# Optimization experiments

Hardware: AMD Instinct MI355X
Metric: run time of the kernel (lower is better)

The kernel has to match this reference:

```python
import jax, jax.numpy as jnp
import numpy as np

N_NODES = 100000
N_EDGES = 3200000
DROP_P = 0.5


def gcn_conv(x, W, b, src, dst, deg_inv_sqrt, n):
    # PyG GCNConv with self-loops already folded into (src, dst):
    # out[j] = sum_{(i->j)} dinv[i]*dinv[j] * (x W)[i] + b
    h = x @ W
    norm = deg_inv_sqrt[src] * deg_inv_sqrt[dst]          # [E+N]
    msg = h[src] * norm[:, None]                          # [E+N, d_out]
    out = jax.ops.segment_sum(msg, dst, num_segments=n)
    return out + b


def dropout(x, key, p=DROP_P):
    keep = jax.random.bernoulli(key, 1.0 - p, x.shape)
    return jnp.where(keep, x / (1.0 - p), 0.0)


def setup_inputs() -> dict:
    key = jax.random.key(0)
    ks = jax.random.split(key, 8)
    x = jax.random.normal(ks[0], (N_NODES, 64), dtype=jnp.float32)
    edge_index = jax.random.randint(ks[1], (2, N_EDGES), 0, N_NODES, dtype=jnp.int64)
    def glorot(k, fin, fout):
        lim = float(np.sqrt(6.0 / (fin + fout)))
        return jax.random.uniform(k, (fin, fout), jnp.float32, -lim, lim)
    return {
        "x": x,
        "edge_index": edge_index,
        "W1": glorot(ks[2], 64, 32), "b1": jnp.zeros((32,), jnp.float32),
        "W2": glorot(ks[3], 32, 64), "b2": jnp.zeros((64,), jnp.float32),
        "W3": glorot(ks[4], 64, 32), "b3": jnp.zeros((32,), jnp.float32),
    }


def reference(x, edge_index, W1, b1, W2, b2, W3, b3):
    n = x.shape[0]
    loops = jnp.arange(n, dtype=edge_index.dtype)
    src = jnp.concatenate([edge_index[0], loops])          # [E+N]
    dst = jnp.concatenate([edge_index[1], loops])
    deg = jax.ops.segment_sum(jnp.ones_like(dst, dtype=x.dtype), dst, num_segments=n)
    deg_inv_sqrt = jnp.where(deg > 0, jax.lax.rsqrt(deg), 0.0)

    dkey = jax.random.key(42)
    k1, k2 = jax.random.split(dkey)

    h = gcn_conv(x, W1, b1, src, dst, deg_inv_sqrt, n)
    h = jax.nn.celu(h)
    h = dropout(h, k1)
    h = gcn_conv(h, W2, b2, src, dst, deg_inv_sqrt, n)
    h = jax.nn.celu(h)
    h = dropout(h, k2)
    h = gcn_conv(h, W3, b3, src, dst, deg_inv_sqrt, n)
    return jax.nn.celu(h)
```

## Files before the change

### kernel.cpp

```cpp
#include <hip/hip_runtime.h>
#include <stdint.h>
#include <stddef.h>

typedef _Float16 half_t;
typedef _Float16 half4 __attribute__((ext_vector_type(4)));
typedef _Float16 half8 __attribute__((ext_vector_type(8)));

__host__ __device__ __forceinline__ uint32_t rotl32(uint32_t v, uint32_t r) {
  return (v << r) | (v >> (32u - r));
}

__host__ __device__ __forceinline__ void tf2x32(uint32_t k0, uint32_t k1,
                                                uint32_t x0, uint32_t x1,
                                                uint32_t& o0, uint32_t& o1) {
  uint32_t ks2 = k0 ^ k1 ^ 0x1BD11BDAu;
  x0 += k0; x1 += k1;
  x0 += x1; x1 = rotl32(x1, 13); x1 ^= x0;
  x0 += x1; x1 = rotl32(x1, 15); x1 ^= x0;
  x0 += x1; x1 = rotl32(x1, 26); x1 ^= x0;
  x0 += x1; x1 = rotl32(x1, 6);  x1 ^= x0;
  x0 += k1; x1 += ks2 + 1u;
  x0 += x1; x1 = rotl32(x1, 17); x1 ^= x0;
  x0 += x1; x1 = rotl32(x1, 29); x1 ^= x0;
  x0 += x1; x1 = rotl32(x1, 16); x1 ^= x0;
  x0 += x1; x1 = rotl32(x1, 24); x1 ^= x0;
  x0 += ks2; x1 += k0 + 2u;
  x0 += x1; x1 = rotl32(x1, 13); x1 ^= x0;
  x0 += x1; x1 = rotl32(x1, 15); x1 ^= x0;
  x0 += x1; x1 = rotl32(x1, 26); x1 ^= x0;
  x0 += x1; x1 = rotl32(x1, 6);  x1 ^= x0;
  x0 += k0; x1 += k1 + 3u;
  x0 += x1; x1 = rotl32(x1, 17); x1 ^= x0;
  x0 += x1; x1 = rotl32(x1, 29); x1 ^= x0;
  x0 += x1; x1 = rotl32(x1, 16); x1 ^= x0;
  x0 += x1; x1 = rotl32(x1, 24); x1 ^= x0;
  x0 += k1; x1 += ks2 + 4u;
  x0 += x1; x1 = rotl32(x1, 13); x1 ^= x0;
  x0 += x1; x1 = rotl32(x1, 15); x1 ^= x0;
  x0 += x1; x1 = rotl32(x1, 26); x1 ^= x0;
  x0 += x1; x1 = rotl32(x1, 6);  x1 ^= x0;
  x0 += ks2; x1 += k0 + 5u;
  o0 = x0; o1 = x1;
}

__device__ __forceinline__ bool tf_keep(uint32_t k0, uint32_t k1, uint32_t idx) {
  uint32_t o0, o1;
  tf2x32(k0, k1, 0u, idx, o0, o1);
  return ((o0 ^ o1) >> 31) == 0u;
}

#define CHUNK 4096
#define STASH 5120

__global__ __launch_bounds__(1024) void zero1024(uint32_t* __restrict__ p) {
  p[threadIdx.x] = 0u;
}

__global__ __launch_bounds__(256) void k4_binhist(const int* __restrict__ src,
                                                  const int* __restrict__ dst,
                                                  uint32_t* __restrict__ tbl,
                                                  uint32_t* __restrict__ gbcnt,
                                                  uint32_t* __restrict__ staging,
                                                  int E, int NB) {
  __shared__ uint32_t lcur[1024];
  __shared__ uint32_t ls[256];
  __shared__ uint32_t stage[CHUNK];
  int tid = threadIdx.x;
  for (int i = tid; i < NB; i += 256) lcur[i] = 0u;
  __syncthreads();
  int base = blockIdx.x * CHUNK;
  int end = min(base + CHUNK, E);
  uint32_t dv[16], sv[16];
  int m = 0;
  for (int i = base + tid; i < end; i += 256) {
    dv[m] = (uint32_t)dst[i];
    sv[m] = (uint32_t)src[i];
    ++m;
  }
  for (int q = 0; q < m; ++q) atomicAdd(&lcur[dv[q] >> 7], 1u);
  __syncthreads();
  uint32_t carry = 0u;
  for (int seg = 0; seg < 1024; seg += 256) {
    int i = seg + tid;
    uint32_t v = (i < NB) ? lcur[i] : 0u;
    ls[tid] = v;
    __syncthreads();
    for (int off = 1; off < 256; off <<= 1) {
      uint32_t t = (tid >= off) ? ls[tid - off] : 0u;
      __syncthreads();
      if (tid >= off) ls[tid] += t;
      __syncthreads();
    }
    uint32_t excl = carry + ls[tid] - v;
    if (i < NB) {
      tbl[(size_t)blockIdx.x * NB + i] = (excl << 16) | v;
      if (v) atomicAdd(&gbcnt[i], v);
      lcur[i] = excl;
    }
    carry += ls[255];
    __syncthreads();
  }
  for (int q = 0; q < m; ++q) {
    uint32_t d = dv[q];
    uint32_t p = atomicAdd(&lcur[d >> 7], 1u);
    stage[p] = ((d & 127u) << 17) | sv[q];
  }
  __syncthreads();
  int cnt_total = end - base;
  uint32_t* outp = staging + (size_t)blockIdx.x * CHUNK;
  for (int i = tid; i < cnt_total; i += 256) outp[i] = stage[i];
}

__global__ __launch_bounds__(1024) void k3_bscan(const uint32_t* __restrict__ gbcnt,
                                                 uint32_t* __restrict__ bbase, int NB) {
  __shared__ uint32_t s[1024];
  int i = threadIdx.x;
  uint32_t v = (i < NB) ? gbcnt[i] : 0u;
  s[i] = v;
  __syncthreads();
  for (int off = 1; off < 1024; off <<= 1) {
    uint32_t t = (i >= off) ? s[i - off] : 0u;
    __syncthreads();
    if (i >= off) s[i] += t;
    __syncthreads();
  }
  if (i < NB) bbase[i] = s[i] - v;
}

__global__ __launch_bounds__(256) void k5_fin(
    const uint32_t* __restrict__ staging, const uint32_t* __restrict__ tbl,
    const uint32_t* __restrict__ bbase, uint32_t* __restrict__ rowp,
    float* __restrict__ dinv, uint32_t* __restrict__ esrc,
    int n, int E, int NBLK, int NB) {
  __shared__ uint32_t lpak[1024];
  __shared__ uint32_t P[1025];
  __shared__ uint32_t ls[256];
  __shared__ uint32_t stash[STASH];
  __shared__ uint32_t lc[128];
  __shared__ uint32_t sc[128];
  __shared__ uint32_t lcur[128];
  int tid = threadIdx.x;
  int b = blockIdx.x;
  if (tid < 128) lc[tid] = 0u;
  uint32_t carry = 0u;
  for (int seg = 0; seg < 1024; seg += 256) {
    int i = seg + tid;
    uint32_t packed = (i < NBLK) ? tbl[(size_t)i * NB + b] : 0u;
    lpak[i] = packed;
    uint32_t v = packed & 0xFFFFu;
    ls[tid] = v;
    __syncthreads();
    for (int off = 1; off < 256; off <<= 1) {
      uint32_t t = (tid >= off) ? ls[tid - off] : 0u;
      __syncthreads();
      if (tid >= off) ls[tid] += t;
      __syncthreads();
    }
    P[i] = carry + ls[tid] - v;
    carry += ls[255];
    __syncthreads();
  }
  if (tid == 0) P[NBLK] = carry;
  __syncthreads();
  uint32_t total = P[NBLK];
  for (int i = tid; i < NBLK; i += 256) {
    uint32_t packed = lpak[i];
    uint32_t cnt = packed & 0xFFFFu;
    uint32_t loff = packed >> 16;
    uint32_t p = P[i];
    const uint32_t* run = staging + (size_t)i * CHUNK + loff;
    for (uint32_t t2 = 0; t2 < cnt; ++t2) {
      uint32_t e = run[t2];
      uint32_t q = p + t2;
      if (q < STASH) stash[q] = e;
      atomicAdd(&lc[e >> 17], 1u);
    }
  }
  __syncthreads();
  uint32_t myc = (tid < 128) ? lc[tid] : 0u;
  if (tid < 128) sc[tid] = myc;
  __syncthreads();
  for (int off = 1; off < 128; off <<= 1) {
    uint32_t t = (tid < 128 && tid >= off) ? sc[tid - off] : 0u;
    __syncthreads();
    if (tid < 128 && tid >= off) sc[tid] += t;
    __syncthreads();
  }
  uint32_t s = bbase[b];
  if (tid < 128) {
    uint32_t gstart = s + sc[tid] - myc;
    int node = (b << 7) + tid;
    if (node < n) {
      rowp[node] = gstart;
      dinv[node] = 1.0f / sqrtf((float)(myc + 1u));
    }
    lcur[tid] = gstart;
  }
  if (b == 0 && tid == 0) rowp[n] = (uint32_t)E;
  __syncthreads();
  uint32_t lim = total < (uint32_t)STASH ? total : (uint32_t)STASH;
  for (uint32_t q = tid; q < lim; q += 256) {
    uint32_t e = stash[q];
    uint32_t pos = atomicAdd(&lcur[e >> 17], 1u);
    esrc[pos] = e & 0x1FFFFu;
  }
  if (total > (uint32_t)STASH) {
    for (int i = tid; i < NBLK; i += 256) {
      uint32_t packed = lpak[i];
      uint32_t cnt = packed & 0xFFFFu;
      uint32_t loff = packed >> 16;
      uint32_t p = P[i];
      const uint32_t* run = staging + (size_t)i * CHUNK + loff;
      for (uint32_t t2 = 0; t2 < cnt; ++t2) {
        uint32_t q = p + t2;
        if (q >= (uint32_t)STASH) {
          uint32_t e = run[t2];
          uint32_t pos = atomicAdd(&lcur[e >> 17], 1u);
          esrc[pos] = e & 0x1FFFFu;
        }
      }
    }
  }
}

__global__ __launch_bounds__(256) void gemm_n64_k32(
    const float* __restrict__ X, const float* __restrict__ W,
    const float* __restrict__ dinv, half_t* __restrict__ out16, int n) {
  __shared__ float Ws[64 * 32];
  __shared__ float Xs[32 * 68];
  int tid = threadIdx.x;
  {
    const float4* Wv = (const float4*)W;
    float4* Wsv = (float4*)Ws;
    Wsv[tid] = Wv[tid];
    Wsv[tid + 256] = Wv[tid + 256];
  }
  int row0 = blockIdx.x * 32;
  {
    const float4* Xv = (const float4*)(X + (size_t)row0 * 64);
    int lim = (n - row0) * 16;
    float4 z = make_float4(0.f, 0.f, 0.f, 0.f);
    int i0 = tid, i1 = tid + 256;
    float4 v0 = (i0 < lim) ? Xv[i0] : z;
    float4 v1 = (i1 < lim) ? Xv[i1] : z;
    *(float4*)(Xs + (i0 >> 4) * 68 + ((i0 & 15) << 2)) = v0;
    *(float4*)(Xs + (i1 >> 4) * 68 + ((i1 & 15) << 2)) = v1;
  }
  __syncthreads();
  int r = tid >> 3;
  int c4 = (tid & 7) << 2;
  int row = row0 + r;
  if (row >= n) return;
  float4 acc = make_float4(0.f, 0.f, 0.f, 0.f);
#pragma unroll
  for (int k = 0; k < 64; k += 4) {
    float4 xv = *(const float4*)(Xs + r * 68 + k);
    float4 w0 = *(const float4*)(Ws + (k + 0) * 32 + c4);
    float4 w1 = *(const float4*)(Ws + (k + 1) * 32 + c4);
    float4 w2 = *(const float4*)(Ws + (k + 2) * 32 + c4);
    float4 w3 = *(const float4*)(Ws + (k + 3) * 32 + c4);
    acc.x = fmaf(xv.x, w0.x, acc.x); acc.y = fmaf(xv.x, w0.y, acc.y);
    acc.z = fmaf(xv.x, w0.z, acc.z); acc.w = fmaf(xv.x, w0.w, acc.w);
    acc.x = fmaf(xv.y, w1.x, acc.x); acc.y = fmaf(xv.y, w1.y, acc.y);
    acc.z = fmaf(xv.y, w1.z, acc.z); acc.w = fmaf(xv.y, w1.w, acc.w);
    acc.x = fmaf(xv.z, w2.x, acc.x); acc.y = fmaf(xv.z, w2.y, acc.y);
    acc.z = fmaf(xv.z, w2.z, acc.z); acc.w = fmaf(xv.z, w2.w, acc.w);
    acc.x = fmaf(xv.w, w3.x, acc.x); acc.y = fmaf(xv.w, w3.y, acc.y);
    acc.z = fmaf(xv.w, w3.z, acc.z); acc.w = fmaf(xv.w, w3.w, acc.w);
  }
  float dj = dinv[row];
  half4 h;
  h.x = (half_t)(acc.x * dj); h.y = (half_t)(acc.y * dj);
  h.z = (half_t)(acc.z * dj); h.w = (half_t)(acc.w * dj);
  *(half4*)(out16 + (size_t)row * 32 + c4) = h;
}

__global__ __launch_bounds__(256) void gemm_k32_n64_act(
    const float* __restrict__ X, const float* __restrict__ W,
    const float* __restrict__ bias, float* __restrict__ out,
    uint32_t k0, uint32_t k1, int n) {
  __shared__ float Ws[32 * 64];
  __shared__ float Xs[16 * 36];
  int tid = threadIdx.x;
  {
    const float4* Wv = (const float4*)W;
    float4* Wsv = (float4*)Ws;
    Wsv[tid] = Wv[tid];
    Wsv[tid + 256] = Wv[tid + 256];
  }
  int row0 = blockIdx.x * 16;
  if (tid < 128) {
    const float4* Xv = (const float4*)(X + (size_t)row0 * 32);
    int lim = (n - row0) * 8;
    float4 z = make_float4(0.f, 0.f, 0.f, 0.f);
    float4 v = (tid < lim) ? Xv[tid] : z;
    *(float4*)(Xs + (tid >> 3) * 36 + ((tid & 7) << 2)) = v;
  }
  __syncthreads();
  int r = tid >> 4;
  int c4 = (tid & 15) << 2;
  int row = row0 + r;
  if (row >= n) return;
  float4 acc = make_float4(0.f, 0.f, 0.f, 0.f);
#pragma unroll
  for (int k = 0; k < 32; k += 4) {
    float4 xv = *(const float4*)(Xs + r * 36 + k);
    float4 w0 = *(const float4*)(Ws + (k + 0) * 64 + c4);
    float4 w1 = *(const float4*)(Ws + (k + 1) * 64 + c4);
    float4 w2 = *(const float4*)(Ws + (k + 2) * 64 + c4);
    float4 w3 = *(const float4*)(Ws + (k + 3) * 64 + c4);
    acc.x = fmaf(xv.x, w0.x, acc.x); acc.y = fmaf(xv.x, w0.y, acc.y);
    acc.z = fmaf(xv.x, w0.z, acc.z); acc.w = fmaf(xv.x, w0.w, acc.w);
    acc.x = fmaf(xv.y, w1.x, acc.x); acc.y = fmaf(xv.y, w1.y, acc.y);
    acc.z = fmaf(xv.y, w1.z, acc.z); acc.w = fmaf(xv.y, w1.w, acc.w);
    acc.x = fmaf(xv.z, w2.x, acc.x); acc.y = fmaf(xv.z, w2.y, acc.y);
    acc.z = fmaf(xv.z, w2.z, acc.z); acc.w = fmaf(xv.z, w2.w, acc.w);
    acc.x = fmaf(xv.w, w3.x, acc.x); acc.y = fmaf(xv.w, w3.y, acc.y);
    acc.z = fmaf(xv.w, w3.z, acc.z); acc.w = fmaf(xv.w, w3.w, acc.w);
  }
  float4 bv = *(const float4*)(bias + c4);
  float vv[4] = {acc.x + bv.x, acc.y + bv.y, acc.z + bv.z, acc.w + bv.w};
  uint32_t base = (uint32_t)row * 64u + (uint32_t)c4;
#pragma unroll
  for (int q = 0; q < 4; ++q) {
    float v = vv[q];
    v = v > 0.f ? v : expm1f(v);
    vv[q] = tf_keep(k0, k1, base + q) ? v * 2.f : 0.f;
  }
  *(float4*)(out + (size_t)row * 64 + c4) = make_float4(vv[0], vv[1], vv[2], vv[3]);
}

__global__ __launch_bounds__(256) void gather_fin(
    const half_t* __restrict__ hs, const uint32_t* __restrict__ rowp,
    const uint32_t* __restrict__ esrc, const float* __restrict__ dinv,
    const float* __restrict__ bias, float* __restrict__ outf,
    half_t* __restrict__ outh, int n, int mode, uint32_t k0, uint32_t k1,
    float fone) {
  __shared__ __align__(16) float ldsred[256];
  int tid = threadIdx.x;
  int gt = blockIdx.x * 256 + tid;
  int j = gt >> 5;
  int g = tid >> 5;
  int l = tid & 31;
  int eslot = l >> 2;
  int chunk = l & 3;
  float acc[8] = {0.f, 0.f, 0.f, 0.f, 0.f, 0.f, 0.f, 0.f};
  uint32_t e0 = 0, deg = 0;
  if (j < n) {
    e0 = rowp[j];
    deg = rowp[j + 1] - e0;
  }
  const half_t* hp = hs + (size_t)(chunk << 3);
  uint32_t base = 0;
  for (; base + 32 <= deg; base += 32) {
    uint32_t idx = esrc[e0 + base + (uint32_t)l];
#pragma unroll
    for (int k = 0; k < 32; k += 8) {
      uint32_t s = (uint32_t)__shfl((int)idx, k + eslot, 32);
      const half8 v = *(const half8*)(hp + ((size_t)s << 5));
#pragma unroll
      for (int q = 0; q < 8; ++q) acc[q] = fmaf((float)v[q], fone, acc[q]);
    }
  }
  if (base < deg) {
    uint32_t rem = deg - base;
    uint32_t li = (uint32_t)l < rem ? (uint32_t)l : rem - 1u;
    uint32_t idx = esrc[e0 + base + li];
    for (uint32_t k = 0; k < rem; k += 8) {
      uint32_t kk = k + (uint32_t)eslot;
      uint32_t ks = kk < rem ? kk : rem - 1u;
      uint32_t s = (uint32_t)__shfl((int)idx, (int)ks, 32);
      if (kk < rem) {
        const half8 v = *(const half8*)(hp + ((size_t)s << 5));
#pragma unroll
        for (int q = 0; q < 8; ++q) acc[q] = fmaf((float)v[q], fone, acc[q]);
      }
    }
  }
#pragma unroll
  for (int m = 4; m <= 16; m <<= 1) {
#pragma unroll
    for (int q = 0; q < 8; ++q) acc[q] += __shfl_xor(acc[q], m);
  }
  if (l < 4) {
    *(float4*)(&ldsred[(g << 5) + (chunk << 3) + 0]) =
        make_float4(acc[0], acc[1], acc[2], acc[3]);
    *(float4*)(&ldsred[(g << 5) + (chunk << 3) + 4]) =
        make_float4(acc[4], acc[5], acc[6], acc[7]);
  }
  __builtin_amdgcn_wave_barrier();
  if (j >= n) return;
  float sum = ldsred[(g << 5) + l];
  sum += (float)hs[(size_t)j * 32 + l];
  float dj = dinv[j];
  float v = dj * sum;
  if (mode == 1) {
    v += bias[l];
    v = v > 0.f ? v : expm1f(v);
    outf[gt] = v;
  } else if (mode == 3) {
    v += bias[l];
    v = v > 0.f ? v : expm1f(v);
    v = tf_keep(k0, k1, (uint32_t)gt) ? v * 2.f : 0.f;
    v *= dj;
    outh[gt] = (half_t)v;
  } else {
    outf[gt] = v;
  }
}

extern "C" void kernel_launch(void* const* d_in, const int* in_sizes, int n_in,
                              void* d_out, int out_size, void* d_ws, size_t ws_size,
                              hipStream_t stream) {
  const float* x  = (const float*)d_in[0];
  const int*   ei = (const int*)d_in[1];
  const float* W1 = (const float*)d_in[2];
  const float* b1 = (const float*)d_in[3];
  const float* W2 = (const float*)d_in[4];
  const float* b2 = (const float*)d_in[5];
  const float* W3 = (const float*)d_in[6];
  const float* b3 = (const float*)d_in[7];
  float* out = (float*)d_out;

  const int n = in_sizes[0] / 64;
  const int E = in_sizes[1] / 2;
  const int* src = ei;
  const int* dst = ei + E;

  char* ws = (char*)d_ws;
  size_t off = 0;
  auto alloc = [&](size_t bytes) {
    void* p = ws + off;
    off = (off + bytes + 255) & ~(size_t)255;
    return p;
  };
  float*    A32   = (float*)alloc((size_t)n * 32 * 4);
  float*    C     = (float*)alloc((size_t)n * 64 * 4);
  half_t*   A16   = (half_t*)alloc((size_t)n * 32 * 2);
  half_t*   B16   = (half_t*)alloc((size_t)n * 32 * 2);
  float*    dinv  = (float*)alloc((size_t)n * 4);
  uint32_t* rowp  = (uint32_t*)alloc((size_t)(n + 1) * 4);
  uint32_t* esrc  = (uint32_t*)alloc((size_t)E * 4);
  uint32_t* gbcnt = (uint32_t*)alloc(1024 * 4);
  uint32_t* bbase = (uint32_t*)alloc(1024 * 4);
  uint32_t* staging = (uint32_t*)C;
  uint32_t* tbl     = (uint32_t*)A32;
  (void)ws_size; (void)n_in; (void)out_size;

  uint32_t k1a, k1b, k2a, k2b;
  tf2x32(0u, 42u, 0u, 0u, k1a, k1b);
  tf2x32(0u, 42u, 0u, 1u, k2a, k2b);

  const int NB   = (n + 127) >> 7;
  const int NBLK = (E + CHUNK - 1) / CHUNK;
  const int nv   = n * 32;
  const int gV   = (nv + 255) / 256;
  const int gG1  = (n + 31) / 32;
  const int gG2  = (n + 15) / 16;
  dim3 blk(256);

  zero1024<<<1, dim3(1024), 0, stream>>>(gbcnt);
  k4_binhist<<<NBLK, blk, 0, stream>>>(src, dst, tbl, gbcnt, staging, E, NB);
  k3_bscan<<<1, dim3(1024), 0, stream>>>(gbcnt, bbase, NB);
  k5_fin<<<NB, blk, 0, stream>>>(staging, tbl, bbase, rowp, dinv, esrc, n, E, NBLK, NB);

  gemm_n64_k32<<<gG1, blk, 0, stream>>>(x, W1, dinv, A16, n);
  gather_fin<<<gV, blk, 0, stream>>>(A16, rowp, esrc, dinv, b1, nullptr, B16, n, 3, k1a, k1b, 1.0f);

  gather_fin<<<gV, blk, 0, stream>>>(B16, rowp, esrc, dinv, nullptr, A32, nullptr, n, 0, 0u, 0u, 1.0f);
  gemm_k32_n64_act<<<gG2, blk, 0, stream>>>(A32, W2, b2, C, k2a, k2b, n);

  gemm_n64_k32<<<gG1, blk, 0, stream>>>(C, W3, dinv, A16, n);
  gather_fin<<<gV, blk, 0, stream>>>(A16, rowp, esrc, dinv, b3, out, nullptr, n, 1, 0u, 0u, 1.0f);
}
```

Before: 334.5 us.

## Widen CSR finalize kernel to 1024 threads with per-edge binary-search gather

The CSR-building finalize kernel now runs 1024 threads per block and does a single 1024-wide prefix scan over chunk counts instead of four 256-wide segmented scans. Edges are no longer copied run by run per chunk. Each thread takes flat edge indices and finds the source chunk with a binary search over the prefix array. This spreads the load evenly across threads and avoids the imbalance from variable run lengths. In exchange it pays a log(NBLK) shared-memory search per edge and assumes NBLK fits in 1024.

```diff
diff --git a/kernel.cpp b/kernel.cpp
--- a/kernel.cpp
+++ b/kernel.cpp
@@ -127,14 +127,14 @@
   if (i < NB) bbase[i] = s[i] - v;
 }
 
-__global__ __launch_bounds__(256) void k5_fin(
+__global__ __launch_bounds__(1024) void k5_fin(
     const uint32_t* __restrict__ staging, const uint32_t* __restrict__ tbl,
     const uint32_t* __restrict__ bbase, uint32_t* __restrict__ rowp,
     float* __restrict__ dinv, uint32_t* __restrict__ esrc,
     int n, int E, int NBLK, int NB) {
-  __shared__ uint32_t lpak[1024];
+  __shared__ uint32_t loff[1024];
   __shared__ uint32_t P[1025];
-  __shared__ uint32_t ls[256];
+  __shared__ uint32_t ls[1024];
   __shared__ uint32_t stash[STASH];
   __shared__ uint32_t lc[128];
   __shared__ uint32_t sc[128];
@@ -142,39 +142,30 @@
   int tid = threadIdx.x;
   int b = blockIdx.x;
   if (tid < 128) lc[tid] = 0u;
-  uint32_t carry = 0u;
-  for (int seg = 0; seg < 1024; seg += 256) {
-    int i = seg + tid;
-    uint32_t packed = (i < NBLK) ? tbl[(size_t)i * NB + b] : 0u;
-    lpak[i] = packed;
-    uint32_t v = packed & 0xFFFFu;
-    ls[tid] = v;
-    __syncthreads();
-    for (int off = 1; off < 256; off <<= 1) {
-      uint32_t t = (tid >= off) ? ls[tid - off] : 0u;
-      __syncthreads();
-      if (tid >= off) ls[tid] += t;
-      __syncthreads();
-    }
-    P[i] = carry + ls[tid] - v;
-    carry += ls[255];
-    __syncthreads();
-  }
-  if (tid == 0) P[NBLK] = carry;
+  uint32_t packed = (tid < NBLK) ? tbl[(size_t)tid * NB + b] : 0u;
+  uint32_t v = packed & 0xFFFFu;
+  loff[tid] = packed >> 16;
+  ls[tid] = v;
+  __syncthreads();
+  for (int off = 1; off < 1024; off <<= 1) {
+    uint32_t t = (tid >= off) ? ls[tid - off] : 0u;
+    __syncthreads();
+    if (tid >= off) ls[tid] += t;
+    __syncthreads();
+  }
+  P[tid] = ls[tid] - v;
+  if (tid == 1023) P[1024] = ls[1023];
   __syncthreads();
   uint32_t total = P[NBLK];
-  for (int i = tid; i < NBLK; i += 256) {
-    uint32_t packed = lpak[i];
-    uint32_t cnt = packed & 0xFFFFu;
-    uint32_t loff = packed >> 16;
-    uint32_t p = P[i];
-    const uint32_t* run = staging + (size_t)i * CHUNK + loff;
-    for (uint32_t t2 = 0; t2 < cnt; ++t2) {
-      uint32_t e = run[t2];
-      uint32_t q = p + t2;
-      if (q < STASH) stash[q] = e;
-      atomicAdd(&lc[e >> 17], 1u);
-    }
+  for (uint32_t q = (uint32_t)tid; q < total; q += 1024u) {
+    int lo = 0, hi = NBLK;
+    while (hi - lo > 1) {
+      int mid = (lo + hi) >> 1;
+      if (P[mid] <= q) lo = mid; else hi = mid;
+    }
+    uint32_t e = staging[(size_t)lo * CHUNK + loff[lo] + (q - P[lo])];
+    if (q < (uint32_t)STASH) stash[q] = e;
+    atomicAdd(&lc[e >> 17], 1u);
   }
   __syncthreads();
   uint32_t myc = (tid < 128) ? lc[tid] : 0u;
@@ -199,26 +190,21 @@
   if (b == 0 && tid == 0) rowp[n] = (uint32_t)E;
   __syncthreads();
   uint32_t lim = total < (uint32_t)STASH ? total : (uint32_t)STASH;
-  for (uint32_t q = tid; q < lim; q += 256) {
+  for (uint32_t q = (uint32_t)tid; q < lim; q += 1024u) {
     uint32_t e = stash[q];
     uint32_t pos = atomicAdd(&lcur[e >> 17], 1u);
     esrc[pos] = e & 0x1FFFFu;
   }
   if (total > (uint32_t)STASH) {
-    for (int i = tid; i < NBLK; i += 256) {
-      uint32_t packed = lpak[i];
-      uint32_t cnt = packed & 0xFFFFu;
-      uint32_t loff = packed >> 16;
-      uint32_t p = P[i];
-      const uint32_t* run = staging + (size_t)i * CHUNK + loff;
-      for (uint32_t t2 = 0; t2 < cnt; ++t2) {
-        uint32_t q = p + t2;
-        if (q >= (uint32_t)STASH) {
-          uint32_t e = run[t2];
-          uint32_t pos = atomicAdd(&lcur[e >> 17], 1u);
-          esrc[pos] = e & 0x1FFFFu;
-        }
+    for (uint32_t q = (uint32_t)STASH + (uint32_t)tid; q < total; q += 1024u) {
+      int lo = 0, hi = NBLK;
+      while (hi - lo > 1) {
+        int mid = (lo + hi) >> 1;
+        if (P[mid] <= q) lo = mid; else hi = mid;
       }
+      uint32_t e = staging[(size_t)lo * CHUNK + loff[lo] + (q - P[lo])];
+      uint32_t pos = atomicAdd(&lcur[e >> 17], 1u);
+      esrc[pos] = e & 0x1FFFFu;
     }
   }
 }
@@ -462,7 +448,7 @@
   zero1024<<<1, dim3(1024), 0, stream>>>(gbcnt);
   k4_binhist<<<NBLK, blk, 0, stream>>>(src, dst, tbl, gbcnt, staging, E, NB);
   k3_bscan<<<1, dim3(1024), 0, stream>>>(gbcnt, bbase, NB);
-  k5_fin<<<NB, blk, 0, stream>>>(staging, tbl, bbase, rowp, dinv, esrc, n, E, NBLK, NB);
+  k5_fin<<<NB, dim3(1024), 0, stream>>>(staging, tbl, bbase, rowp, dinv, esrc, n, E, NBLK, NB);
 
   gemm_n64_k32<<<gG1, blk, 0, stream>>>(x, W1, dinv, A16, n);
   gather_fin<<<gV, blk, 0, stream>>>(A16, rowp, esrc, dinv, b1, nullptr, B16, n, 3, k1a, k1b, 1.0f);
```

New measurement: 329.3 us. Within noise of the previous version (-1.5%).
